# Optimization experiments

Measured on AMD Instinct MI355X. Metric: run time of the kernel, lower is better.

The kernel has to match this reference:

```python
import jax, jax.numpy as jnp
import numpy as np

N = 50000      # nodes
E = 800000     # random edges (self-loops appended -> E + N total)
IN, HID, OUT, HEADS = 128, 256, 256, 8


def _gat_layer(x, src, dst, W, a_src, a_dst, bias):
    # x: [N, F_in]; W: [F_in, H*C]; a_src/a_dst: [H, C]; bias: [H*C]
    n = x.shape[0]
    H, C = a_src.shape
    h = (x @ W).reshape(n, H, C)                      # per-head transform
    al_s = jnp.sum(h * a_src, axis=-1)                # [N, H]
    al_d = jnp.sum(h * a_dst, axis=-1)                # [N, H]
    e = jax.nn.leaky_relu(al_s[src] + al_d[dst], 0.2) # [E, H]
    # segmented softmax over incoming edges of each destination node
    m = jax.ops.segment_max(e, dst, num_segments=n)   # [N, H]
    e = jnp.exp(e - m[dst])
    s = jax.ops.segment_sum(e, dst, num_segments=n)   # [N, H]
    alpha = e / (s[dst] + 1e-16)                      # [E, H]
    out = jax.ops.segment_sum(alpha[:, :, None] * h[src], dst, num_segments=n)
    return out.reshape(n, H * C) + bias


def setup_inputs() -> dict:
    key = jax.random.key(0)
    ks = jax.random.split(key, 9)
    x = jax.random.normal(ks[0], (N, IN), dtype=jnp.float32)
    src = jax.random.randint(ks[1], (E,), 0, N)
    dst = jax.random.randint(ks[2], (E,), 0, N)
    loop = jnp.arange(N)  # PyG GATConv adds self-loops by default
    edge_index = jnp.stack([jnp.concatenate([src, loop]),
                            jnp.concatenate([dst, loop])]).astype(jnp.int64)
    C1, C2 = HID // HEADS, OUT // HEADS
    W1 = jax.random.normal(ks[3], (IN, HID), jnp.float32) * (1.0 / np.sqrt(IN))
    a1_src = jax.random.normal(ks[4], (HEADS, C1), jnp.float32) * 0.1
    a1_dst = jax.random.normal(ks[5], (HEADS, C1), jnp.float32) * 0.1
    b1 = jnp.zeros((HID,), jnp.float32)
    W2 = jax.random.normal(ks[6], (HID, OUT), jnp.float32) * (1.0 / np.sqrt(HID))
    a2_src = jax.random.normal(ks[7], (HEADS, C2), jnp.float32) * 0.1
    a2_dst = jax.random.normal(ks[8], (HEADS, C2), jnp.float32) * 0.1
    b2 = jnp.zeros((OUT,), jnp.float32)
    return {"x": x, "edge_index": edge_index,
            "W1": W1, "a1_src": a1_src, "a1_dst": a1_dst, "b1": b1,
            "W2": W2, "a2_src": a2_src, "a2_dst": a2_dst, "b2": b2}


def reference(x, edge_index, W1, a1_src, a1_dst, b1, W2, a2_src, a2_dst, b2):
    src, dst = edge_index[0], edge_index[1]
    h = jax.nn.elu(_gat_layer(x, src, dst, W1, a1_src, a1_dst, b1))
    out = jax.nn.elu(_gat_layer(h, src, dst, W2, a2_src, a2_dst, b2))
    return out
```

## Files before the change

### kernel.cpp

```cpp
#include <hip/hip_runtime.h>
#include <hip/hip_bf16.h>


#define HEADS 8
#define F 256

typedef _Float16 h8 __attribute__((ext_vector_type(8)));
typedef _Float16 h4 __attribute__((ext_vector_type(4)));
typedef float f4 __attribute__((ext_vector_type(4)));

#define WAVE_SYNC() do { __builtin_amdgcn_wave_barrier(); \
  asm volatile("s_waitcnt lgkmcnt(0)" ::: "memory"); \
  __builtin_amdgcn_wave_barrier(); } while (0)


__global__ void k_cvt(const float* __restrict__ in, _Float16* __restrict__ out, int n) {
  int i = blockIdx.x * blockDim.x + threadIdx.x;
  int idx = i * 4;
  if (idx < n) {
    float4 v = *(const float4*)&in[idx];
    h4 o = {(_Float16)v.x, (_Float16)v.y, (_Float16)v.z, (_Float16)v.w};
    *(h4*)&out[idx] = o;
  }
}

__global__ void k_cvt_wt(const float* __restrict__ W, _Float16* __restrict__ Wt, int K) {
  int k = blockIdx.x, n = threadIdx.x;
  Wt[(size_t)n * K + k] = (_Float16)W[(size_t)k * F + n];
}


__global__ void k_hist(const int* __restrict__ dst, int Et, int* __restrict__ deg) {
  int i = blockIdx.x * blockDim.x + threadIdx.x;
  if (i < Et) atomicAdd(&deg[dst[i]], 1);
}

__global__ __launch_bounds__(1024) void k_scan1(const int* __restrict__ deg, int n,
                                                int* __restrict__ rowptr, int* __restrict__ bsum) {
  __shared__ int s[1024];
  int i = blockIdx.x * 1024 + threadIdx.x;
  int v = (i < n) ? deg[i] : 0;
  s[threadIdx.x] = v;
  __syncthreads();
  for (int off = 1; off < 1024; off <<= 1) {
    int add = (threadIdx.x >= off) ? s[threadIdx.x - off] : 0;
    __syncthreads();
    s[threadIdx.x] += add;
    __syncthreads();
  }
  if (i < n) rowptr[i] = s[threadIdx.x] - v;
  if (threadIdx.x == 1023) bsum[blockIdx.x] = s[1023];
}

__global__ void k_scan2(const int* __restrict__ bsum, int nb, int* __restrict__ boff) {
  int t = threadIdx.x;
  int v = (t < nb) ? bsum[t] : 0;
  int inc = v;
  for (int off = 1; off < 64; off <<= 1) {
    int y = __shfl_up(inc, off, 64);
    if (t >= off) inc += y;
  }
  boff[t] = inc - v;
}

__global__ void k_scan3(int n, int Et, int* __restrict__ rowptr, const int* __restrict__ boff) {
  int i = blockIdx.x * blockDim.x + threadIdx.x;
  if (i < n) rowptr[i] += boff[i >> 10];
  if (i == 0) rowptr[n] = Et;
}

__global__ void k_fill(const int* __restrict__ src, const int* __restrict__ dst, int Et,
                       const int* __restrict__ rowptr, int* __restrict__ fill,
                       int* __restrict__ csr_src) {
  int i = blockIdx.x * blockDim.x + threadIdx.x;
  if (i < Et) {
    int d = dst[i];
    int pos = rowptr[d] + atomicAdd(&fill[d], 1);
    csr_src[pos] = src[i];
  }
}


__global__ __launch_bounds__(256) void k_gemm(const _Float16* __restrict__ A,
                                              const _Float16* __restrict__ Bt,
                                              _Float16* __restrict__ C,
                                              const float* __restrict__ a_src,
                                              const float* __restrict__ a_dst,
                                              float* __restrict__ als,
                                              float* __restrict__ ald,
                                              int M, int K) {
  __shared__ _Float16 As[64][40];
  __shared__ _Float16 Bs[64][40];
  int tid = threadIdx.x;
  int lane = tid & 63, wid = tid >> 6;
  int wr = wid >> 1, wc = wid & 1;
  int rowBase = blockIdx.x * 64, colBase = blockIdx.y * 64;
  f4 acc[2][2] = {};

  int srow = tid >> 2;
  int skoff = (tid & 3) * 8;
  int arow_g = min(rowBase + srow, M - 1);
  const _Float16* Ap = A + (size_t)arow_g * K + skoff;
  const _Float16* Bp = Bt + (size_t)(colBase + srow) * K + skoff;

  int kl = (lane >> 4) * 8;
  int rl = lane & 15;

  for (int k0 = 0; k0 < K; k0 += 32) {
    h8 av = *(const h8*)(Ap + k0);
    h8 bv = *(const h8*)(Bp + k0);
    *(h8*)&As[srow][skoff] = av;
    *(h8*)&Bs[srow][skoff] = bv;
    __syncthreads();
    h8 a0 = *(const h8*)&As[wr * 32 + rl][kl];
    h8 a1 = *(const h8*)&As[wr * 32 + 16 + rl][kl];
    h8 b0 = *(const h8*)&Bs[wc * 32 + rl][kl];
    h8 b1 = *(const h8*)&Bs[wc * 32 + 16 + rl][kl];
    acc[0][0] = __builtin_amdgcn_mfma_f32_16x16x32_f16(a0, b0, acc[0][0], 0, 0, 0);
    acc[0][1] = __builtin_amdgcn_mfma_f32_16x16x32_f16(a0, b1, acc[0][1], 0, 0, 0);
    acc[1][0] = __builtin_amdgcn_mfma_f32_16x16x32_f16(a1, b0, acc[1][0], 0, 0, 0);
    acc[1][1] = __builtin_amdgcn_mfma_f32_16x16x32_f16(a1, b1, acc[1][1], 0, 0, 0);
    __syncthreads();
  }

  int colL = lane & 15;
  int rquad = (lane >> 4) * 4;

#pragma unroll
  for (int fi = 0; fi < 2; ++fi)
#pragma unroll
    for (int fj = 0; fj < 2; ++fj) {
      int col = colBase + wc * 32 + fj * 16 + colL;
#pragma unroll
      for (int r = 0; r < 4; ++r) {
        int row = rowBase + wr * 32 + fi * 16 + rquad + r;
        if (row < M) C[(size_t)row * F + col] = (_Float16)acc[fi][fj][r];
      }
    }

  int head = blockIdx.y * 2 + wc;
  float as0 = a_src[head * 32 + colL];
  float as1 = a_src[head * 32 + 16 + colL];
  float ad0 = a_dst[head * 32 + colL];
  float ad1 = a_dst[head * 32 + 16 + colL];
#pragma unroll
  for (int fi = 0; fi < 2; ++fi)
#pragma unroll
    for (int r = 0; r < 4; ++r) {
      float vs = acc[fi][0][r] * as0 + acc[fi][1][r] * as1;
      float vd = acc[fi][0][r] * ad0 + acc[fi][1][r] * ad1;
#pragma unroll
      for (int off = 8; off; off >>= 1) {
        vs += __shfl_xor(vs, off);
        vd += __shfl_xor(vd, off);
      }
      int row = rowBase + wr * 32 + fi * 16 + rquad + r;
      if (colL == 0 && row < M) {
        als[row * HEADS + head] = vs;
        ald[row * HEADS + head] = vd;
      }
    }
}


template <bool F16OUT>
__global__ __launch_bounds__(256) void k_agg(const int* __restrict__ rowptr,
                                             const int* __restrict__ csr_src,
                                             const float* __restrict__ al_s,
                                             const float* __restrict__ al_d,
                                             const _Float16* __restrict__ h,
                                             const float* __restrict__ bias,
                                             float* __restrict__ outf,
                                             _Float16* __restrict__ outh,
                                             int n) {
  __shared__ float eps[4][64][8];
  __shared__ int ssrc[4][64];
  int tid = threadIdx.x;
  int w = tid >> 6, lane = tid & 63;
  int node = blockIdx.x * 4 + w;
  if (node >= n) return;
  int base = rowptr[node];
  int d = rowptr[node + 1] - base;
  int hh = lane >> 3, slot = lane & 7;
  float alD = al_d[node * HEADS + hh];

  float invs;
  f4 facc = {0.f, 0.f, 0.f, 0.f};
  const _Float16* hc = h + (lane << 2);

  if (d <= 64) {
    float m = -1e30f;
    for (int j = slot; j < d; j += 8) {
      int s = csr_src[base + j];
      if (hh == 0) ssrc[w][j] = s;
      float e = al_s[s * HEADS + hh] + alD;
      e = (e > 0.f) ? e : 0.2f * e;
      eps[w][j][hh] = e;
      m = fmaxf(m, e);
    }
#pragma unroll
    for (int off = 4; off; off >>= 1) m = fmaxf(m, __shfl_xor(m, off));
    float sm = 0.f;
    for (int j = slot; j < d; j += 8) {
      float p = __expf(eps[w][j][hh] - m);
      eps[w][j][hh] = p;
      sm += p;
    }
#pragma unroll
    for (int off = 4; off; off >>= 1) sm += __shfl_xor(sm, off);
    invs = 1.f / (sm + 1e-16f);
    WAVE_SYNC();
    int j = 0;
    for (; j + 2 <= d; j += 2) {
      int s0 = __builtin_amdgcn_readfirstlane(ssrc[w][j]);
      int s1 = __builtin_amdgcn_readfirstlane(ssrc[w][j + 1]);
      float p0 = eps[w][j][hh], p1 = eps[w][j + 1][hh];
      h4 v0 = *(const h4*)(hc + ((size_t)s0 << 8));
      h4 v1 = *(const h4*)(hc + ((size_t)s1 << 8));
      facc.x += p0 * (float)v0.x + p1 * (float)v1.x;
      facc.y += p0 * (float)v0.y + p1 * (float)v1.y;
      facc.z += p0 * (float)v0.z + p1 * (float)v1.z;
      facc.w += p0 * (float)v0.w + p1 * (float)v1.w;
    }
    if (j < d) {
      int s0 = __builtin_amdgcn_readfirstlane(ssrc[w][j]);
      float p0 = eps[w][j][hh];
      h4 v0 = *(const h4*)(hc + ((size_t)s0 << 8));
      facc.x += p0 * (float)v0.x;
      facc.y += p0 * (float)v0.y;
      facc.z += p0 * (float)v0.z;
      facc.w += p0 * (float)v0.w;
    }
  } else {
    float m = -1e30f;
    for (int j = slot; j < d; j += 8) {
      int s = csr_src[base + j];
      float e = al_s[s * HEADS + hh] + alD;
      e = (e > 0.f) ? e : 0.2f * e;
      m = fmaxf(m, e);
    }
#pragma unroll
    for (int off = 4; off; off >>= 1) m = fmaxf(m, __shfl_xor(m, off));
    float sm = 0.f;
    for (int j = slot; j < d; j += 8) {
      int s = csr_src[base + j];
      float e = al_s[s * HEADS + hh] + alD;
      e = (e > 0.f) ? e : 0.2f * e;
      sm += __expf(e - m);
    }
#pragma unroll
    for (int off = 4; off; off >>= 1) sm += __shfl_xor(sm, off);
    invs = 1.f / (sm + 1e-16f);
    for (int c0 = 0; c0 < d; c0 += 64) {
      int cn = min(64, d - c0);
      WAVE_SYNC();
      for (int j = slot; j < cn; j += 8) {
        int s = csr_src[base + c0 + j];
        if (hh == 0) ssrc[w][j] = s;
        float e = al_s[s * HEADS + hh] + alD;
        e = (e > 0.f) ? e : 0.2f * e;
        eps[w][j][hh] = __expf(e - m);
      }
      WAVE_SYNC();
      for (int j = 0; j < cn; ++j) {
        int s0 = __builtin_amdgcn_readfirstlane(ssrc[w][j]);
        float p0 = eps[w][j][hh];
        h4 v0 = *(const h4*)(hc + ((size_t)s0 << 8));
        facc.x += p0 * (float)v0.x;
        facc.y += p0 * (float)v0.y;
        facc.z += p0 * (float)v0.z;
        facc.w += p0 * (float)v0.w;
      }
    }
  }

  int c0 = lane << 2;
  float4 bv = *(const float4*)&bias[c0];
  float o0 = facc.x * invs + bv.x;
  float o1 = facc.y * invs + bv.y;
  float o2 = facc.z * invs + bv.z;
  float o3 = facc.w * invs + bv.w;
  o0 = (o0 > 0.f) ? o0 : expm1f(o0);
  o1 = (o1 > 0.f) ? o1 : expm1f(o1);
  o2 = (o2 > 0.f) ? o2 : expm1f(o2);
  o3 = (o3 > 0.f) ? o3 : expm1f(o3);
  if (F16OUT) {
    h4 o = {(_Float16)o0, (_Float16)o1, (_Float16)o2, (_Float16)o3};
    *(h4*)&outh[((size_t)node << 8) + c0] = o;
  } else {
    *(float4*)&outf[((size_t)node << 8) + c0] = make_float4(o0, o1, o2, o3);
  }
}


extern "C" void kernel_launch(void* const* d_in, const int* in_sizes, int n_in,
                              void* d_out, int out_size, void* d_ws, size_t ws_size,
                              hipStream_t stream) {
  const float* x   = (const float*)d_in[0];
  const int*   ei  = (const int*)d_in[1];
  const float* W1  = (const float*)d_in[2];
  const float* a1s = (const float*)d_in[3];
  const float* a1d = (const float*)d_in[4];
  const float* b1  = (const float*)d_in[5];
  const float* W2  = (const float*)d_in[6];
  const float* a2s = (const float*)d_in[7];
  const float* a2d = (const float*)d_in[8];
  const float* b2  = (const float*)d_in[9];

  int n  = in_sizes[0] / 128;
  int Et = in_sizes[1] / 2;
  const int* srcp = ei;
  const int* dstp = ei + Et;

  char* ws = (char*)d_ws;
  auto alloc = [&](size_t bytes) {
    char* p = ws;
    ws += (bytes + 255) & ~(size_t)255;
    return p;
  };
  _Float16* xh     = (_Float16*)alloc((size_t)n * 128 * 2);
  _Float16* hbuf   = (_Float16*)alloc((size_t)n * F * 2);
  _Float16* Wt1    = (_Float16*)alloc((size_t)128 * F * 2);
  _Float16* Wt2    = (_Float16*)alloc((size_t)F * F * 2);
  float*    als    = (float*)alloc((size_t)n * HEADS * 4);
  float*    ald    = (float*)alloc((size_t)n * HEADS * 4);
  int*      deg    = (int*)alloc((size_t)n * 4);
  int*      fill   = (int*)alloc((size_t)n * 4);
  int*      rowptr = (int*)alloc((size_t)(n + 1) * 4);
  int*      bsum   = (int*)alloc(64 * 4);
  int*      boff   = (int*)alloc(64 * 4);
  int*      csr    = (int*)alloc((size_t)Et * 4);
  _Float16* out1h  = (_Float16*)d_out;
  float*    outF   = (float*)d_out;

  hipMemsetAsync(deg, 0, (size_t)n * 4, stream);
  hipMemsetAsync(fill, 0, (size_t)n * 4, stream);

  k_cvt<<<(n * 128 / 4 + 255) / 256, 256, 0, stream>>>(x, xh, n * 128);
  k_cvt_wt<<<128, 256, 0, stream>>>(W1, Wt1, 128);
  k_cvt_wt<<<256, 256, 0, stream>>>(W2, Wt2, 256);

  int eb = (Et + 255) / 256;
  k_hist<<<eb, 256, 0, stream>>>(dstp, Et, deg);
  int nb = (n + 1023) / 1024;
  k_scan1<<<nb, 1024, 0, stream>>>(deg, n, rowptr, bsum);
  k_scan2<<<1, 64, 0, stream>>>(bsum, nb, boff);
  k_scan3<<<(n + 255) / 256, 256, 0, stream>>>(n, Et, rowptr, boff);
  k_fill<<<eb, 256, 0, stream>>>(srcp, dstp, Et, rowptr, fill, csr);

  dim3 gg((n + 63) / 64, 4);
  int ab = (n + 3) / 4;
  k_gemm<<<gg, 256, 0, stream>>>(xh, Wt1, hbuf, a1s, a1d, als, ald, n, 128);
  k_agg<true><<<ab, 256, 0, stream>>>(rowptr, csr, als, ald, hbuf, b1, nullptr, out1h, n);
  k_gemm<<<gg, 256, 0, stream>>>(out1h, Wt2, hbuf, a2s, a2d, als, ald, n, 256);
  k_agg<false><<<ab, 256, 0, stream>>>(rowptr, csr, als, ald, hbuf, b2, outF, nullptr, n);
}
```

Before: 393.9 us.

## Compute full 256-column GEMM tile per block and unroll aggregation gather by four

The GEMM now has each block compute a 64x256 output tile, with each wave owning 64 columns and a 4x4 grid of MFMA fragments. The A tile is then loaded once per row block instead of once for each of four column blocks, and the grid drops its second dimension. The attention-logit epilogue now reduces two heads per wave. The aggregation loop is unrolled from 2 to 4 neighbor rows to put more gather loads in flight. In exchange, accumulator register use and shared memory grow, which may lower occupancy, and the grid has a quarter as many blocks.

```diff
diff --git a/kernel.cpp b/kernel.cpp
--- a/kernel.cpp
+++ b/kernel.cpp
@@ -90,74 +90,85 @@
                                               float* __restrict__ ald,
                                               int M, int K) {
   __shared__ _Float16 As[64][40];
-  __shared__ _Float16 Bs[64][40];
+  __shared__ _Float16 Bs[256][40];
   int tid = threadIdx.x;
-  int lane = tid & 63, wid = tid >> 6;
-  int wr = wid >> 1, wc = wid & 1;
-  int rowBase = blockIdx.x * 64, colBase = blockIdx.y * 64;
-  f4 acc[2][2] = {};
-
-  int srow = tid >> 2;
-  int skoff = (tid & 3) * 8;
-  int arow_g = min(rowBase + srow, M - 1);
-  const _Float16* Ap = A + (size_t)arow_g * K + skoff;
-  const _Float16* Bp = Bt + (size_t)(colBase + srow) * K + skoff;
+  int lane = tid & 63, w = tid >> 6;
+  int rowBase = blockIdx.x * 64;
+  f4 acc[4][4] = {};
+
+  int arow = tid >> 2, akoff = (tid & 3) * 8;
+  int arow_g = min(rowBase + arow, M - 1);
+  const _Float16* Ap = A + (size_t)arow_g * K + akoff;
+  const _Float16* Bp = Bt + (size_t)tid * K;
 
   int kl = (lane >> 4) * 8;
   int rl = lane & 15;
 
   for (int k0 = 0; k0 < K; k0 += 32) {
     h8 av = *(const h8*)(Ap + k0);
-    h8 bv = *(const h8*)(Bp + k0);
-    *(h8*)&As[srow][skoff] = av;
-    *(h8*)&Bs[srow][skoff] = bv;
+    h8 bv0 = *(const h8*)(Bp + k0);
+    h8 bv1 = *(const h8*)(Bp + k0 + 8);
+    h8 bv2 = *(const h8*)(Bp + k0 + 16);
+    h8 bv3 = *(const h8*)(Bp + k0 + 24);
+    *(h8*)&As[arow][akoff] = av;
+    *(h8*)&Bs[tid][0] = bv0;
+    *(h8*)&Bs[tid][8] = bv1;
+    *(h8*)&Bs[tid][16] = bv2;
+    *(h8*)&Bs[tid][24] = bv3;
     __syncthreads();
-    h8 a0 = *(const h8*)&As[wr * 32 + rl][kl];
-    h8 a1 = *(const h8*)&As[wr * 32 + 16 + rl][kl];
-    h8 b0 = *(const h8*)&Bs[wc * 32 + rl][kl];
-    h8 b1 = *(const h8*)&Bs[wc * 32 + 16 + rl][kl];
-    acc[0][0] = __builtin_amdgcn_mfma_f32_16x16x32_f16(a0, b0, acc[0][0], 0, 0, 0);
-    acc[0][1] = __builtin_amdgcn_mfma_f32_16x16x32_f16(a0, b1, acc[0][1], 0, 0, 0);
-    acc[1][0] = __builtin_amdgcn_mfma_f32_16x16x32_f16(a1, b0, acc[1][0], 0, 0, 0);
-    acc[1][1] = __builtin_amdgcn_mfma_f32_16x16x32_f16(a1, b1, acc[1][1], 0, 0, 0);
+    h8 af[4], bf[4];
+#pragma unroll
+    for (int fi = 0; fi < 4; ++fi) af[fi] = *(const h8*)&As[fi * 16 + rl][kl];
+#pragma unroll
+    for (int fj = 0; fj < 4; ++fj) bf[fj] = *(const h8*)&Bs[w * 64 + fj * 16 + rl][kl];
+#pragma unroll
+    for (int fi = 0; fi < 4; ++fi)
+#pragma unroll
+      for (int fj = 0; fj < 4; ++fj)
+        acc[fi][fj] = __builtin_amdgcn_mfma_f32_16x16x32_f16(af[fi], bf[fj], acc[fi][fj], 0, 0, 0);
     __syncthreads();
   }
 
-  int colL = lane & 15;
   int rquad = (lane >> 4) * 4;
 
 #pragma unroll
-  for (int fi = 0; fi < 2; ++fi)
-#pragma unroll
-    for (int fj = 0; fj < 2; ++fj) {
-      int col = colBase + wc * 32 + fj * 16 + colL;
+  for (int fi = 0; fi < 4; ++fi)
+#pragma unroll
+    for (int fj = 0; fj < 4; ++fj) {
+      int col = w * 64 + fj * 16 + rl;
 #pragma unroll
       for (int r = 0; r < 4; ++r) {
-        int row = rowBase + wr * 32 + fi * 16 + rquad + r;
+        int row = rowBase + fi * 16 + rquad + r;
         if (row < M) C[(size_t)row * F + col] = (_Float16)acc[fi][fj][r];
       }
     }
 
-  int head = blockIdx.y * 2 + wc;
-  float as0 = a_src[head * 32 + colL];
-  float as1 = a_src[head * 32 + 16 + colL];
-  float ad0 = a_dst[head * 32 + colL];
-  float ad1 = a_dst[head * 32 + 16 + colL];
-#pragma unroll
-  for (int fi = 0; fi < 2; ++fi)
+  int head0 = w * 2;
+  float as0 = a_src[head0 * 32 + rl],      as1 = a_src[head0 * 32 + 16 + rl];
+  float ad0 = a_dst[head0 * 32 + rl],      ad1 = a_dst[head0 * 32 + 16 + rl];
+  float cs0 = a_src[head0 * 32 + 32 + rl], cs1 = a_src[head0 * 32 + 48 + rl];
+  float cd0 = a_dst[head0 * 32 + 32 + rl], cd1 = a_dst[head0 * 32 + 48 + rl];
+#pragma unroll
+  for (int fi = 0; fi < 4; ++fi)
 #pragma unroll
     for (int r = 0; r < 4; ++r) {
-      float vs = acc[fi][0][r] * as0 + acc[fi][1][r] * as1;
-      float vd = acc[fi][0][r] * ad0 + acc[fi][1][r] * ad1;
+      float v0s = acc[fi][0][r] * as0 + acc[fi][1][r] * as1;
+      float v0d = acc[fi][0][r] * ad0 + acc[fi][1][r] * ad1;
+      float v1s = acc[fi][2][r] * cs0 + acc[fi][3][r] * cs1;
+      float v1d = acc[fi][2][r] * cd0 + acc[fi][3][r] * cd1;
 #pragma unroll
       for (int off = 8; off; off >>= 1) {
-        vs += __shfl_xor(vs, off);
-        vd += __shfl_xor(vd, off);
-      }
-      int row = rowBase + wr * 32 + fi * 16 + rquad + r;
-      if (colL == 0 && row < M) {
-        als[row * HEADS + head] = vs;
-        ald[row * HEADS + head] = vd;
+        v0s += __shfl_xor(v0s, off);
+        v0d += __shfl_xor(v0d, off);
+        v1s += __shfl_xor(v1s, off);
+        v1d += __shfl_xor(v1d, off);
+      }
+      int row = rowBase + fi * 16 + rquad + r;
+      if (rl == 0 && row < M) {
+        als[row * HEADS + head0] = v0s;
+        ald[row * HEADS + head0] = v0d;
+        als[row * HEADS + head0 + 1] = v1s;
+        ald[row * HEADS + head0 + 1] = v1d;
       }
     }
 }
@@ -211,18 +222,23 @@
     invs = 1.f / (sm + 1e-16f);
     WAVE_SYNC();
     int j = 0;
-    for (; j + 2 <= d; j += 2) {
+    for (; j + 4 <= d; j += 4) {
       int s0 = __builtin_amdgcn_readfirstlane(ssrc[w][j]);
       int s1 = __builtin_amdgcn_readfirstlane(ssrc[w][j + 1]);
+      int s2 = __builtin_amdgcn_readfirstlane(ssrc[w][j + 2]);
+      int s3 = __builtin_amdgcn_readfirstlane(ssrc[w][j + 3]);
       float p0 = eps[w][j][hh], p1 = eps[w][j + 1][hh];
+      float p2 = eps[w][j + 2][hh], p3 = eps[w][j + 3][hh];
       h4 v0 = *(const h4*)(hc + ((size_t)s0 << 8));
       h4 v1 = *(const h4*)(hc + ((size_t)s1 << 8));
-      facc.x += p0 * (float)v0.x + p1 * (float)v1.x;
-      facc.y += p0 * (float)v0.y + p1 * (float)v1.y;
-      facc.z += p0 * (float)v0.z + p1 * (float)v1.z;
-      facc.w += p0 * (float)v0.w + p1 * (float)v1.w;
-    }
-    if (j < d) {
+      h4 v2 = *(const h4*)(hc + ((size_t)s2 << 8));
+      h4 v3 = *(const h4*)(hc + ((size_t)s3 << 8));
+      facc.x += p0 * (float)v0.x + p1 * (float)v1.x + p2 * (float)v2.x + p3 * (float)v3.x;
+      facc.y += p0 * (float)v0.y + p1 * (float)v1.y + p2 * (float)v2.y + p3 * (float)v3.y;
+      facc.z += p0 * (float)v0.z + p1 * (float)v1.z + p2 * (float)v2.z + p3 * (float)v3.z;
+      facc.w += p0 * (float)v0.w + p1 * (float)v1.w + p2 * (float)v2.w + p3 * (float)v3.w;
+    }
+    for (; j < d; ++j) {
       int s0 = __builtin_amdgcn_readfirstlane(ssrc[w][j]);
       float p0 = eps[w][j][hh];
       h4 v0 = *(const h4*)(hc + ((size_t)s0 << 8));
@@ -348,10 +364,10 @@
   k_scan3<<<(n + 255) / 256, 256, 0, stream>>>(n, Et, rowptr, boff);
   k_fill<<<eb, 256, 0, stream>>>(srcp, dstp, Et, rowptr, fill, csr);
 
-  dim3 gg((n + 63) / 64, 4);
+  int gb = (n + 63) / 64;
   int ab = (n + 3) / 4;
-  k_gemm<<<gg, 256, 0, stream>>>(xh, Wt1, hbuf, a1s, a1d, als, ald, n, 128);
+  k_gemm<<<gb, 256, 0, stream>>>(xh, Wt1, hbuf, a1s, a1d, als, ald, n, 128);
   k_agg<true><<<ab, 256, 0, stream>>>(rowptr, csr, als, ald, hbuf, b1, nullptr, out1h, n);
-  k_gemm<<<gg, 256, 0, stream>>>(out1h, Wt2, hbuf, a2s, a2d, als, ald, n, 256);
+  k_gemm<<<gb, 256, 0, stream>>>(out1h, Wt2, hbuf, a2s, a2d, als, ald, n, 256);
   k_agg<false><<<ab, 256, 0, stream>>>(rowptr, csr, als, ald, hbuf, b2, outF, nullptr, n);
 }
```

New measurement: 395.3 us. About the same (+0.4%).
